# Kernel optimization log

Hardware: AMD Instinct MI355X
Metric: run time of the kernel (lower is better)

The kernel has to match this reference:

```python
import jax, jax.numpy as jnp
import numpy as np

S, B, H = 512, 32, 1024      # seq, batch, hidden_size
L = 4096                      # total spans (flattened ragged labels)
D = 1024                      # label_size (feature dim)
V = 32000                     # vocab size


def setup_inputs() -> dict:
    key = jax.random.key(0)
    ks = jax.random.split(key, 10)
    hidden = jax.random.normal(ks[0], (S, B, H), dtype=jnp.float32)
    span_bid = jax.random.randint(ks[1], (L,), 0, B)
    span_begin = jax.random.randint(ks[2], (L,), 0, S)
    span_end_m1 = jax.random.randint(ks[3], (L,), 0, S)  # (end - 1) index
    tags = jax.random.randint(ks[4], (L,), 0, V)
    # hidden2feature: Linear(2H -> D) with bias, Tanh
    W1 = jax.random.normal(ks[5], (D, 2 * H), dtype=jnp.float32) * (1.0 / np.sqrt(2 * H))
    b1 = jnp.zeros((D,), dtype=jnp.float32)
    # SoftmaxLoss h2o: Linear(D -> V, bias=False)
    Wout = jax.random.normal(ks[6], (V, D), dtype=jnp.float32) * (1.0 / np.sqrt(D))
    # discard probs from synthetic frequency counts
    counts = jax.random.uniform(ks[7], (V,), minval=1e-5, maxval=1.0)
    freqs = counts / counts.sum()
    discard_probs = jnp.clip(1.0 - jnp.sqrt(1e-4 / freqs), 0.0, None)
    return {"hidden": hidden, "W1": W1, "b1": b1, "Wout": Wout,
            "discard_probs": discard_probs, "span_bid": span_bid,
            "span_begin": span_begin, "span_end_m1": span_end_m1, "tags": tags}


def reference(hidden, W1, b1, Wout, discard_probs, span_bid, span_begin, span_end_m1, tags):
    # gather span endpoint embeddings: [L, H] each
    emb_b = hidden[span_begin, span_bid]
    emb_e = hidden[span_end_m1, span_bid]
    span_emb = jnp.concatenate([emb_b, emb_e], axis=-1)          # [L, 2H]
    feat = jnp.tanh(span_emb @ W1.T + b1)                        # [L, D]
    logits = feat @ Wout.T                                       # [L, V]
    logp = jax.nn.log_softmax(logits, axis=-1)
    nll = -jnp.take_along_axis(logp, tags[:, None], axis=-1)[:, 0]  # [L]
    scaled = 1.0 - discard_probs[tags]
    n_tags = tags.shape[0]
    return jnp.sum(nll * scaled) / (n_tags + 1e-5)
```

## Files before the change

kernel.cpp:

```cpp
#include <hip/hip_runtime.h>
#include <hip/hip_bf16.h>

#define LSPANS 4096
#define BB 32
#define HH 1024
#define DD 1024
#define VV 32000
#define K1 2048
#define NT2 250

typedef unsigned short u16;
typedef __attribute__((ext_vector_type(8))) short bf16x8v;
typedef __attribute__((ext_vector_type(4))) float f32x4v;

__device__ __forceinline__ u16 f2bf(float x) {
  union { float f; unsigned u; } v; v.f = x;
  unsigned r = (v.u >> 16) & 1u;
  return (u16)((v.u + 0x7fffu + r) >> 16);
}

__global__ void prep1_kernel(const float* __restrict__ hidden,
                             const int* __restrict__ bid,
                             const int* __restrict__ sb,
                             const int* __restrict__ se,
                             u16* __restrict__ A1,
                             const float* __restrict__ W1,
                             u16* __restrict__ W1b) {
  const int blk = blockIdx.x;
  if (blk < LSPANS) {
    const int l = blk;
    const int t = threadIdx.x;
    const int b = bid[l];
    const float* p0 = hidden + ((size_t)sb[l] * BB + b) * HH;
    const float* p1 = hidden + ((size_t)se[l] * BB + b) * HH;
    u16* dst = A1 + (size_t)l * K1;
    float4 v0 = ((const float4*)p0)[t];
    float4 v1 = ((const float4*)p1)[t];
    ushort4 o0; o0.x = f2bf(v0.x); o0.y = f2bf(v0.y); o0.z = f2bf(v0.z); o0.w = f2bf(v0.w);
    ushort4 o1; o1.x = f2bf(v1.x); o1.y = f2bf(v1.y); o1.z = f2bf(v1.z); o1.w = f2bf(v1.w);
    ((ushort4*)dst)[t]          = o0;
    ((ushort4*)(dst + HH))[t]   = o1;
  } else {
    const int n4 = DD * K1 / 4;
    int i = (blk - LSPANS) * 256 + threadIdx.x;
    const int stride = 512 * 256;
    for (; i < n4; i += stride) {
      float4 v = ((const float4*)W1)[i];
      ushort4 o;
      o.x = f2bf(v.x); o.y = f2bf(v.y); o.z = f2bf(v.z); o.w = f2bf(v.w);
      ((ushort4*)W1b)[i] = o;
    }
  }
}

__launch_bounds__(256, 2)
__global__ void prep2_kernel(const u16* __restrict__ A, const u16* __restrict__ B,
                             const float* __restrict__ bias,
                             u16* __restrict__ feat_out,
                             const float* __restrict__ Wout,
                             u16* __restrict__ Woutb) {
  __shared__ __align__(16) u16 As[128 * 64];
  __shared__ __align__(16) u16 Bs[64 * 64];

  if (blockIdx.x < 512) {
    const int tid  = threadIdx.x;
    const int lane = tid & 63;
    const int w    = tid >> 6;
    const int wm   = w & 1;
    const int wn   = w >> 1;
    const int q    = lane >> 4;
    const int lm   = lane & 15;
    const int mBase = (blockIdx.x & 31) * 128;
    const int nBase = (blockIdx.x >> 5) * 64;

    f32x4v acc[4][2];
#pragma unroll
    for (int i = 0; i < 4; ++i)
#pragma unroll
      for (int j = 0; j < 2; ++j) acc[i][j] = (f32x4v){0.f, 0.f, 0.f, 0.f};

    const int srowA = w * 32 + (lane >> 3);
    const int srowB = w * 16 + (lane >> 3);
    const int scol  = ((lane & 7) ^ (lane >> 3)) * 8;
    const u16* Ag = A + (size_t)(mBase + srowA) * K1 + scol;
    const u16* Bg = B + (size_t)(nBase + srowB) * K1 + scol;

    for (int k0 = 0; k0 < K1; k0 += 64) {
#pragma unroll
      for (int c = 0; c < 4; ++c) {
        __builtin_amdgcn_global_load_lds(
            (const __attribute__((address_space(1))) void*)(Ag + k0 + (size_t)c * 8 * K1),
            (__attribute__((address_space(3))) void*)(As + (w * 32 + c * 8) * 64), 16, 0, 0);
      }
#pragma unroll
      for (int c = 0; c < 2; ++c) {
        __builtin_amdgcn_global_load_lds(
            (const __attribute__((address_space(1))) void*)(Bg + k0 + (size_t)c * 8 * K1),
            (__attribute__((address_space(3))) void*)(Bs + (w * 16 + c * 8) * 64), 16, 0, 0);
      }
      __syncthreads();
#pragma unroll
      for (int kk = 0; kk < 64; kk += 32) {
        bf16x8v af[4], bfr[2];
        const int sw = lm & 7;
#pragma unroll
        for (int i = 0; i < 4; ++i) {
          int row = wm * 64 + i * 16 + lm;
          int kch = (kk >> 3) + q;
          af[i] = *(const bf16x8v*)(As + row * 64 + ((kch ^ sw) << 3));
        }
#pragma unroll
        for (int j = 0; j < 2; ++j) {
          int row = wn * 32 + j * 16 + lm;
          int kch = (kk >> 3) + q;
          bfr[j] = *(const bf16x8v*)(Bs + row * 64 + ((kch ^ sw) << 3));
        }
#pragma unroll
        for (int i = 0; i < 4; ++i)
#pragma unroll
          for (int j = 0; j < 2; ++j)
            acc[i][j] = __builtin_amdgcn_mfma_f32_16x16x32_bf16(af[i], bfr[j], acc[i][j], 0, 0, 0);
      }
      __syncthreads();
    }

    float bj[2];
#pragma unroll
    for (int j = 0; j < 2; ++j) bj[j] = bias[nBase + wn * 32 + j * 16 + lm];
#pragma unroll
    for (int i = 0; i < 4; ++i)
#pragma unroll
      for (int j = 0; j < 2; ++j)
#pragma unroll
        for (int r = 0; r < 4; ++r) {
          int tr = wm * 64 + i * 16 + q * 4 + r;
          int tc = wn * 32 + j * 16 + lm;
          float v = tanhf(acc[i][j][r] + bj[j]);
          feat_out[(size_t)(mBase + tr) * DD + nBase + tc] = f2bf(v);
        }
  } else {
    const int n4 = VV * DD / 4;
    int i = (blockIdx.x - 512) * 256 + threadIdx.x;
    const int stride = 2048 * 256;
    for (; i < n4; i += stride) {
      float4 v = ((const float4*)Wout)[i];
      ushort4 o;
      o.x = f2bf(v.x); o.y = f2bf(v.y); o.z = f2bf(v.z); o.w = f2bf(v.w);
      ((ushort4*)Woutb)[i] = o;
    }
  }
}

__launch_bounds__(256, 2)
__global__ void gemm2_kernel(const u16* __restrict__ A, const u16* __restrict__ B,
                             const int* __restrict__ tags,
                             float* __restrict__ pmax, float* __restrict__ psum,
                             float* __restrict__ ltag) {
  __shared__ __align__(16) u16 As[128 * 64];
  __shared__ __align__(16) u16 Bs[128 * 64];
  __shared__ float rmax[2][128];
  __shared__ float rsum[2][128];
  __shared__ int   stags[128];

  const int tid  = threadIdx.x;
  const int lane = tid & 63;
  const int w    = tid >> 6;
  const int wm   = w & 1;
  const int wn   = w >> 1;
  const int q    = lane >> 4;
  const int lm   = lane & 15;
  const int mBase = blockIdx.x * 128;
  const int nBase = blockIdx.y * 128;

  if (tid < 128) stags[tid] = tags[mBase + tid];

  f32x4v acc[4][4];
#pragma unroll
  for (int i = 0; i < 4; ++i)
#pragma unroll
    for (int j = 0; j < 4; ++j) acc[i][j] = (f32x4v){0.f, 0.f, 0.f, 0.f};

  const int srow = w * 32 + (lane >> 3);
  const int scol = ((lane & 7) ^ (lane >> 3)) * 8;
  const u16* Ag = A + (size_t)(mBase + srow) * DD + scol;
  const u16* Bg = B + (size_t)(nBase + srow) * DD + scol;

  for (int k0 = 0; k0 < DD; k0 += 64) {
#pragma unroll
    for (int c = 0; c < 4; ++c) {
      __builtin_amdgcn_global_load_lds(
          (const __attribute__((address_space(1))) void*)(Ag + k0 + (size_t)c * 8 * DD),
          (__attribute__((address_space(3))) void*)(As + (w * 32 + c * 8) * 64), 16, 0, 0);
    }
#pragma unroll
    for (int c = 0; c < 4; ++c) {
      __builtin_amdgcn_global_load_lds(
          (const __attribute__((address_space(1))) void*)(Bg + k0 + (size_t)c * 8 * DD),
          (__attribute__((address_space(3))) void*)(Bs + (w * 32 + c * 8) * 64), 16, 0, 0);
    }
    __syncthreads();
#pragma unroll
    for (int kk = 0; kk < 64; kk += 32) {
      bf16x8v af[4], bfr[4];
      const int sw = lm & 7;
#pragma unroll
      for (int i = 0; i < 4; ++i) {
        int row = wm * 64 + i * 16 + lm;
        int kch = (kk >> 3) + q;
        af[i] = *(const bf16x8v*)(As + row * 64 + ((kch ^ sw) << 3));
      }
#pragma unroll
      for (int j = 0; j < 4; ++j) {
        int row = wn * 64 + j * 16 + lm;
        int kch = (kk >> 3) + q;
        bfr[j] = *(const bf16x8v*)(Bs + row * 64 + ((kch ^ sw) << 3));
      }
#pragma unroll
      for (int i = 0; i < 4; ++i)
#pragma unroll
        for (int j = 0; j < 4; ++j)
          acc[i][j] = __builtin_amdgcn_mfma_f32_16x16x32_bf16(af[i], bfr[j], acc[i][j], 0, 0, 0);
    }
    __syncthreads();
  }

#pragma unroll
  for (int i = 0; i < 4; ++i)
#pragma unroll
    for (int r = 0; r < 4; ++r) {
      float m = fmaxf(fmaxf(acc[i][0][r], acc[i][1][r]),
                      fmaxf(acc[i][2][r], acc[i][3][r]));
#pragma unroll
      for (int off = 1; off < 16; off <<= 1) m = fmaxf(m, __shfl_xor(m, off, 64));
      if (lm == 0) rmax[wn][wm * 64 + i * 16 + q * 4 + r] = m;
    }
  __syncthreads();
#pragma unroll
  for (int i = 0; i < 4; ++i)
#pragma unroll
    for (int r = 0; r < 4; ++r) {
      int tr = wm * 64 + i * 16 + q * 4 + r;
      float M = fmaxf(rmax[0][tr], rmax[1][tr]);
      float s = __expf(acc[i][0][r] - M) + __expf(acc[i][1][r] - M) +
                __expf(acc[i][2][r] - M) + __expf(acc[i][3][r] - M);
#pragma unroll
      for (int off = 1; off < 16; off <<= 1) s += __shfl_xor(s, off, 64);
      if (lm == 0) rsum[wn][tr] = s;
    }
  __syncthreads();
  if (tid < 128) {
    float M = fmaxf(rmax[0][tid], rmax[1][tid]);
    float S = rsum[0][tid] + rsum[1][tid];
    pmax[(size_t)blockIdx.y * LSPANS + mBase + tid] = M;
    psum[(size_t)blockIdx.y * LSPANS + mBase + tid] = S;
  }
#pragma unroll
  for (int i = 0; i < 4; ++i)
#pragma unroll
    for (int r = 0; r < 4; ++r) {
      int tr = wm * 64 + i * 16 + q * 4 + r;
      int tg = stags[tr];
#pragma unroll
      for (int j = 0; j < 4; ++j) {
        int gc = nBase + wn * 64 + j * 16 + lm;
        if (tg == gc) ltag[mBase + tr] = acc[i][j][r];
      }
    }
}

__global__ void finalize_kernel(const float* __restrict__ pmax, const float* __restrict__ psum,
                                const float* __restrict__ ltag, const int* __restrict__ tags,
                                const float* __restrict__ dprob, float* __restrict__ out) {
  const int lane = threadIdx.x & 63;
  const int wv   = threadIdx.x >> 6;
  const int row  = blockIdx.x * 64 + lane;

  float M = -1e30f, S = 0.f;
  for (int t = wv; t < NT2; t += 4) {
    float pm = pmax[(size_t)t * LSPANS + row];
    float ps = psum[(size_t)t * LSPANS + row];
    float Mn = fmaxf(M, pm);
    S = S * __expf(M - Mn) + ps * __expf(pm - Mn);
    M = Mn;
  }

  __shared__ float lmax[4][64];
  __shared__ float lsum[4][64];
  lmax[wv][lane] = M;
  lsum[wv][lane] = S;
  __syncthreads();

  if (wv == 0) {
    float M0 = fmaxf(fmaxf(lmax[0][lane], lmax[1][lane]),
                     fmaxf(lmax[2][lane], lmax[3][lane]));
    float S0 = lsum[0][lane] * __expf(lmax[0][lane] - M0)
             + lsum[1][lane] * __expf(lmax[1][lane] - M0)
             + lsum[2][lane] * __expf(lmax[2][lane] - M0)
             + lsum[3][lane] * __expf(lmax[3][lane] - M0);
    float nll = M0 + logf(S0) - ltag[row];
    float wgt = 1.0f - dprob[tags[row]];
    float val = nll * wgt * (1.0f / (4096.0f + 1e-5f));
#pragma unroll
    for (int off = 1; off < 64; off <<= 1) val += __shfl_xor(val, off, 64);
    if (lane == 0) atomicAdd(out, val);
  }
}

extern "C" void kernel_launch(void* const* d_in, const int* in_sizes, int n_in,
                              void* d_out, int out_size, void* d_ws, size_t ws_size,
                              hipStream_t stream) {
  const float* hidden = (const float*)d_in[0];
  const float* W1     = (const float*)d_in[1];
  const float* b1     = (const float*)d_in[2];
  const float* Wout   = (const float*)d_in[3];
  const float* dprob  = (const float*)d_in[4];
  const int*   bid    = (const int*)d_in[5];
  const int*   sb     = (const int*)d_in[6];
  const int*   se     = (const int*)d_in[7];
  const int*   tags   = (const int*)d_in[8];
  float* out = (float*)d_out;

  char* ws = (char*)d_ws;
  u16* A1    = (u16*)ws;                 ws += (size_t)LSPANS * K1 * 2;
  u16* W1b   = (u16*)ws;                 ws += (size_t)DD * K1 * 2;
  u16* Woutb = (u16*)ws;                 ws += (size_t)VV * DD * 2;
  u16* feat  = (u16*)ws;                 ws += (size_t)LSPANS * DD * 2;
  float* pmax = (float*)ws;              ws += (size_t)NT2 * LSPANS * 4;
  float* psum = (float*)ws;              ws += (size_t)NT2 * LSPANS * 4;
  float* ltag = (float*)ws;              ws += (size_t)LSPANS * 4;

  hipMemsetAsync(d_out, 0, sizeof(float), stream);

  prep1_kernel<<<LSPANS + 512, 256, 0, stream>>>(hidden, bid, sb, se, A1, W1, W1b);

  prep2_kernel<<<512 + 2048, 256, 0, stream>>>(A1, W1b, b1, feat, Wout, Woutb);

  gemm2_kernel<<<dim3(LSPANS / 128, NT2), 256, 0, stream>>>(
      feat, Woutb, tags, pmax, psum, ltag);

  finalize_kernel<<<LSPANS / 64, 256, 0, stream>>>(pmax, psum, ltag, tags, dprob, out);
}
```

Before: 605.4 us.

## Quantize feat and Wout to FP8 and use scaled 32x32x64 FP8 MFMA

```diff
diff --git a/kernel.cpp b/kernel.cpp
--- a/kernel.cpp
+++ b/kernel.cpp
@@ -10,8 +10,12 @@
 #define NT2 250
 
 typedef unsigned short u16;
+typedef unsigned char u8;
 typedef __attribute__((ext_vector_type(8))) short bf16x8v;
 typedef __attribute__((ext_vector_type(4))) float f32x4v;
+typedef __attribute__((ext_vector_type(16))) float f32x16v;
+typedef __attribute__((ext_vector_type(4))) int i32x4v;
+typedef __attribute__((ext_vector_type(8))) int i32x8v;
 
 __device__ __forceinline__ u16 f2bf(float x) {
   union { float f; unsigned u; } v; v.f = x;
@@ -56,9 +60,9 @@
 __launch_bounds__(256, 2)
 __global__ void prep2_kernel(const u16* __restrict__ A, const u16* __restrict__ B,
                              const float* __restrict__ bias,
-                             u16* __restrict__ feat_out,
+                             u8* __restrict__ feat_out,
                              const float* __restrict__ Wout,
-                             u16* __restrict__ Woutb) {
+                             u8* __restrict__ Woutb) {
   __shared__ __align__(16) u16 As[128 * 64];
   __shared__ __align__(16) u16 Bs[64 * 64];
 
@@ -135,8 +139,9 @@
         for (int r = 0; r < 4; ++r) {
           int tr = wm * 64 + i * 16 + q * 4 + r;
           int tc = wn * 32 + j * 16 + lm;
-          float v = tanhf(acc[i][j][r] + bj[j]);
-          feat_out[(size_t)(mBase + tr) * DD + nBase + tc] = f2bf(v);
+          float v = tanhf(acc[i][j][r] + bj[j]) * 64.0f;
+          int p = __builtin_amdgcn_cvt_pk_fp8_f32(v, v, 0, false);
+          feat_out[(size_t)(mBase + tr) * DD + nBase + tc] = (u8)(p & 0xFF);
         }
   } else {
     const int n4 = VV * DD / 4;
@@ -144,20 +149,21 @@
     const int stride = 2048 * 256;
     for (; i < n4; i += stride) {
       float4 v = ((const float4*)Wout)[i];
-      ushort4 o;
-      o.x = f2bf(v.x); o.y = f2bf(v.y); o.z = f2bf(v.z); o.w = f2bf(v.w);
-      ((ushort4*)Woutb)[i] = o;
+      int p = 0;
+      p = __builtin_amdgcn_cvt_pk_fp8_f32(v.x * 16.0f, v.y * 16.0f, p, false);
+      p = __builtin_amdgcn_cvt_pk_fp8_f32(v.z * 16.0f, v.w * 16.0f, p, true);
+      ((int*)Woutb)[i] = p;
     }
   }
 }
 
 __launch_bounds__(256, 2)
-__global__ void gemm2_kernel(const u16* __restrict__ A, const u16* __restrict__ B,
+__global__ void gemm2_kernel(const u8* __restrict__ A, const u8* __restrict__ B,
                              const int* __restrict__ tags,
                              float* __restrict__ pmax, float* __restrict__ psum,
                              float* __restrict__ ltag) {
-  __shared__ __align__(16) u16 As[128 * 64];
-  __shared__ __align__(16) u16 Bs[128 * 64];
+  __shared__ __align__(16) u8 As[128 * 128];
+  __shared__ __align__(16) u8 Bs[128 * 128];
   __shared__ float rmax[2][128];
   __shared__ float rsum[2][128];
   __shared__ int   stags[128];
@@ -167,85 +173,95 @@
   const int w    = tid >> 6;
   const int wm   = w & 1;
   const int wn   = w >> 1;
-  const int q    = lane >> 4;
-  const int lm   = lane & 15;
+  const int l5   = lane >> 5;
+  const int lr   = lane & 31;
+  const int sw   = lr & 7;
   const int mBase = blockIdx.x * 128;
   const int nBase = blockIdx.y * 128;
 
   if (tid < 128) stags[tid] = tags[mBase + tid];
 
-  f32x4v acc[4][4];
-#pragma unroll
-  for (int i = 0; i < 4; ++i)
-#pragma unroll
-    for (int j = 0; j < 4; ++j) acc[i][j] = (f32x4v){0.f, 0.f, 0.f, 0.f};
+  f32x16v acc[2][2];
+#pragma unroll
+  for (int i = 0; i < 2; ++i)
+#pragma unroll
+    for (int j = 0; j < 2; ++j)
+#pragma unroll
+      for (int r = 0; r < 16; ++r) acc[i][j][r] = 0.f;
 
   const int srow = w * 32 + (lane >> 3);
-  const int scol = ((lane & 7) ^ (lane >> 3)) * 8;
-  const u16* Ag = A + (size_t)(mBase + srow) * DD + scol;
-  const u16* Bg = B + (size_t)(nBase + srow) * DD + scol;
-
-  for (int k0 = 0; k0 < DD; k0 += 64) {
+  const int scol = ((lane & 7) ^ (lane >> 3)) * 16;
+  const u8* Ag = A + (size_t)(mBase + srow) * DD + scol;
+  const u8* Bg = B + (size_t)(nBase + srow) * DD + scol;
+
+  const int arow = (wm * 64 + lr) * 128;
+  const int brow = (wn * 64 + lr) * 128;
+
+  for (int k0 = 0; k0 < DD; k0 += 128) {
 #pragma unroll
     for (int c = 0; c < 4; ++c) {
       __builtin_amdgcn_global_load_lds(
           (const __attribute__((address_space(1))) void*)(Ag + k0 + (size_t)c * 8 * DD),
-          (__attribute__((address_space(3))) void*)(As + (w * 32 + c * 8) * 64), 16, 0, 0);
+          (__attribute__((address_space(3))) void*)(As + (w * 32 + c * 8) * 128), 16, 0, 0);
     }
 #pragma unroll
     for (int c = 0; c < 4; ++c) {
       __builtin_amdgcn_global_load_lds(
           (const __attribute__((address_space(1))) void*)(Bg + k0 + (size_t)c * 8 * DD),
-          (__attribute__((address_space(3))) void*)(Bs + (w * 32 + c * 8) * 64), 16, 0, 0);
+          (__attribute__((address_space(3))) void*)(Bs + (w * 32 + c * 8) * 128), 16, 0, 0);
     }
     __syncthreads();
 #pragma unroll
-    for (int kk = 0; kk < 64; kk += 32) {
-      bf16x8v af[4], bfr[4];
-      const int sw = lm & 7;
-#pragma unroll
-      for (int i = 0; i < 4; ++i) {
-        int row = wm * 64 + i * 16 + lm;
-        int kch = (kk >> 3) + q;
-        af[i] = *(const bf16x8v*)(As + row * 64 + ((kch ^ sw) << 3));
-      }
-#pragma unroll
-      for (int j = 0; j < 4; ++j) {
-        int row = wn * 64 + j * 16 + lm;
-        int kch = (kk >> 3) + q;
-        bfr[j] = *(const bf16x8v*)(Bs + row * 64 + ((kch ^ sw) << 3));
-      }
-#pragma unroll
-      for (int i = 0; i < 4; ++i)
-#pragma unroll
-        for (int j = 0; j < 4; ++j)
-          acc[i][j] = __builtin_amdgcn_mfma_f32_16x16x32_bf16(af[i], bfr[j], acc[i][j], 0, 0, 0);
+    for (int kk = 0; kk < 2; ++kk) {
+      const int cb = kk * 4 + l5 * 2;
+      const int o0 = ((cb ^ sw) << 4);
+      const int o1 = (((cb + 1) ^ sw) << 4);
+      i32x8v af[2], bfv[2];
+#pragma unroll
+      for (int i = 0; i < 2; ++i) {
+        const u8* p = As + arow + i * 4096;
+        i32x4v lo = *(const i32x4v*)(p + o0);
+        i32x4v hi = *(const i32x4v*)(p + o1);
+        af[i] = __builtin_shufflevector(lo, hi, 0, 1, 2, 3, 4, 5, 6, 7);
+      }
+#pragma unroll
+      for (int j = 0; j < 2; ++j) {
+        const u8* p = Bs + brow + j * 4096;
+        i32x4v lo = *(const i32x4v*)(p + o0);
+        i32x4v hi = *(const i32x4v*)(p + o1);
+        bfv[j] = __builtin_shufflevector(lo, hi, 0, 1, 2, 3, 4, 5, 6, 7);
+      }
+#pragma unroll
+      for (int i = 0; i < 2; ++i)
+#pragma unroll
+        for (int j = 0; j < 2; ++j)
+          acc[i][j] = __builtin_amdgcn_mfma_scale_f32_32x32x64_f8f6f4(
+              af[i], bfv[j], acc[i][j], 0, 0, 0, 0x7F, 0, 0x7F);
     }
     __syncthreads();
   }
 
-#pragma unroll
-  for (int i = 0; i < 4; ++i)
-#pragma unroll
-    for (int r = 0; r < 4; ++r) {
-      float m = fmaxf(fmaxf(acc[i][0][r], acc[i][1][r]),
-                      fmaxf(acc[i][2][r], acc[i][3][r]));
-#pragma unroll
-      for (int off = 1; off < 16; off <<= 1) m = fmaxf(m, __shfl_xor(m, off, 64));
-      if (lm == 0) rmax[wn][wm * 64 + i * 16 + q * 4 + r] = m;
+  const float SC = 0.0009765625f;
+#pragma unroll
+  for (int i = 0; i < 2; ++i)
+#pragma unroll
+    for (int r = 0; r < 16; ++r) {
+      float m = fmaxf(acc[i][0][r], acc[i][1][r]);
+#pragma unroll
+      for (int off = 1; off < 32; off <<= 1) m = fmaxf(m, __shfl_xor(m, off, 64));
+      if (lr == 0) rmax[wn][wm * 64 + i * 32 + ((r & 3) + 8 * (r >> 2) + 4 * l5)] = m * SC;
     }
   __syncthreads();
 #pragma unroll
-  for (int i = 0; i < 4; ++i)
-#pragma unroll
-    for (int r = 0; r < 4; ++r) {
-      int tr = wm * 64 + i * 16 + q * 4 + r;
+  for (int i = 0; i < 2; ++i)
+#pragma unroll
+    for (int r = 0; r < 16; ++r) {
+      int tr = wm * 64 + i * 32 + ((r & 3) + 8 * (r >> 2) + 4 * l5);
       float M = fmaxf(rmax[0][tr], rmax[1][tr]);
-      float s = __expf(acc[i][0][r] - M) + __expf(acc[i][1][r] - M) +
-                __expf(acc[i][2][r] - M) + __expf(acc[i][3][r] - M);
-#pragma unroll
-      for (int off = 1; off < 16; off <<= 1) s += __shfl_xor(s, off, 64);
-      if (lm == 0) rsum[wn][tr] = s;
+      float s = __expf(acc[i][0][r] * SC - M) + __expf(acc[i][1][r] * SC - M);
+#pragma unroll
+      for (int off = 1; off < 32; off <<= 1) s += __shfl_xor(s, off, 64);
+      if (lr == 0) rsum[wn][tr] = s;
     }
   __syncthreads();
   if (tid < 128) {
@@ -255,15 +271,15 @@
     psum[(size_t)blockIdx.y * LSPANS + mBase + tid] = S;
   }
 #pragma unroll
-  for (int i = 0; i < 4; ++i)
-#pragma unroll
-    for (int r = 0; r < 4; ++r) {
-      int tr = wm * 64 + i * 16 + q * 4 + r;
+  for (int i = 0; i < 2; ++i)
+#pragma unroll
+    for (int r = 0; r < 16; ++r) {
+      int tr = wm * 64 + i * 32 + ((r & 3) + 8 * (r >> 2) + 4 * l5);
       int tg = stags[tr];
 #pragma unroll
-      for (int j = 0; j < 4; ++j) {
-        int gc = nBase + wn * 64 + j * 16 + lm;
-        if (tg == gc) ltag[mBase + tr] = acc[i][j][r];
+      for (int j = 0; j < 2; ++j) {
+        int gc = nBase + wn * 64 + j * 32 + lr;
+        if (tg == gc) ltag[mBase + tr] = acc[i][j][r] * SC;
       }
     }
 }
@@ -323,8 +339,8 @@
   char* ws = (char*)d_ws;
   u16* A1    = (u16*)ws;                 ws += (size_t)LSPANS * K1 * 2;
   u16* W1b   = (u16*)ws;                 ws += (size_t)DD * K1 * 2;
-  u16* Woutb = (u16*)ws;                 ws += (size_t)VV * DD * 2;
-  u16* feat  = (u16*)ws;                 ws += (size_t)LSPANS * DD * 2;
+  u8*  Woutb = (u8*)ws;                  ws += (size_t)VV * DD;
+  u8*  feat  = (u8*)ws;                  ws += (size_t)LSPANS * DD;
   float* pmax = (float*)ws;              ws += (size_t)NT2 * LSPANS * 4;
   float* psum = (float*)ws;              ws += (size_t)NT2 * LSPANS * 4;
   float* ltag = (float*)ws;              ws += (size_t)LSPANS * 4;
```

Result: slower. 1.000 ms (+65.2%).
